# Performance work log

Hardware: AMD Instinct MI355X
Metric: run time of the kernel (lower is better)

Reference implementation:

```python
import jax, jax.numpy as jnp
import numpy as np

# DeformConv hyperparameters (from init_kwargs)
KH, KW = 3, 3
STRIDE, PAD, DIL = 1, 1, 1
GROUPS, DG = 1, 1  # groups=1, deformable_groups=1
B, C, H, W = 4, 64, 128, 128
O = 64
HO = (H + 2 * PAD - (DIL * (KH - 1) + 1)) // STRIDE + 1  # 128
WO = (W + 2 * PAD - (DIL * (KW - 1) + 1)) // STRIDE + 1  # 128


def setup_inputs() -> dict:
    key = jax.random.key(0)
    k1, k2, k3, k4 = jax.random.split(key, 4)
    x = jax.random.normal(k1, (B, C, H, W), dtype=jnp.float32)
    # offset channels: dg * K * 2, ordered (y, x) per kernel tap (DCNv1 CUDA layout)
    offset = jax.random.normal(k2, (B, 2 * DG * KH * KW, HO, WO), dtype=jnp.float32)
    fan_in = C * KH * KW
    weight = jax.random.normal(k3, (O, C // GROUPS, KH, KW), dtype=jnp.float32) / np.sqrt(fan_in)
    bias = jax.random.normal(k4, (O,), dtype=jnp.float32) * 0.01
    return {"x": x, "offset": offset, "weight": weight, "bias": bias}


def _deform_sample(x, offset):
    """Bilinear-sample x at deformed kernel tap locations.
    Returns [B, C, K, HO, WO] where K = KH*KW."""
    K = KH * KW
    Cg = C // DG
    # offset -> [B, DG, K, 2, HO, WO]; channel layout: dg*2*K, pairs (y, x)
    off = offset.reshape(B, DG, K, 2, HO, WO)
    off_y, off_x = off[:, :, :, 0], off[:, :, :, 1]  # [B, DG, K, HO, WO]

    ki = (jnp.arange(K) // KW).astype(jnp.float32)  # kernel row
    kj = (jnp.arange(K) % KW).astype(jnp.float32)   # kernel col
    base_h = (jnp.arange(HO) * STRIDE - PAD).astype(jnp.float32)
    base_w = (jnp.arange(WO) * STRIDE - PAD).astype(jnp.float32)

    # sampling positions [B, DG, K, HO, WO]
    py = off_y + (ki * DIL)[None, None, :, None, None] + base_h[None, None, None, :, None]
    px = off_x + (kj * DIL)[None, None, :, None, None] + base_w[None, None, None, None, :]

    y0f = jnp.floor(py)
    x0f = jnp.floor(px)
    ly = py - y0f
    lx = px - x0f
    hy = 1.0 - ly
    hx = 1.0 - lx
    y0 = y0f.astype(jnp.int32)
    x0 = x0f.astype(jnp.int32)
    y1 = y0 + 1
    x1 = x0 + 1

    flat = x.reshape(B, DG, Cg, H * W)

    def gather(yi, xi, wgt):
        valid = (yi >= 0) & (yi < H) & (xi >= 0) & (xi < W)
        idx = jnp.clip(yi, 0, H - 1) * W + jnp.clip(xi, 0, W - 1)
        idx = idx.reshape(B, DG, 1, K * HO * WO)
        v = jnp.take_along_axis(flat, idx, axis=-1).reshape(B, DG, Cg, K, HO, WO)
        return v * (wgt * valid.astype(wgt.dtype))[:, :, None]

    val = (gather(y0, x0, hy * hx) + gather(y0, x1, hy * lx)
           + gather(y1, x0, ly * hx) + gather(y1, x1, ly * lx))
    return val.reshape(B, C, K, HO, WO)


def reference(x, offset, weight, bias):
    sampled = _deform_sample(x, offset)              # [B, C, K, HO, WO]
    w = weight.reshape(O, C, KH * KW)                # groups = 1
    out = jnp.einsum('bckhw,ock->bohw', sampled, w)  # im2col + GEMM
    return out + bias[None, :, None, None]
```

## Files before the change

kernel.cpp:

```cpp
#include <hip/hip_runtime.h>
#include <hip/hip_fp16.h>


#define B_  4
#define C_  64
#define H_  128
#define W_  128
#define O_  64
#define HO_ 128
#define WO_ 128
#define NCHUNK 8
#define NGW 12
#define KSTEPS 3
#define NT_ 32
#define NTASK (9 * NT_)
#define SG  10
#define SBUF (SG * NT_ * 8)

typedef _Float16 half8 __attribute__((ext_vector_type(8)));
typedef __attribute__((ext_vector_type(4))) float f32x4;

union H8 { float4 v; __half2 h2[4]; half8 v8; };

__global__ __launch_bounds__(256)
void prep(const float* __restrict__ x, const float* __restrict__ w,
          __half* __restrict__ xt, __half* __restrict__ wt) {
    const int tid = threadIdx.x;
    if (blockIdx.x < 2048) {
        int t = blockIdx.x * 256 + tid;
        int xc = t & 127;
        int y  = (t >> 7) & 127;
        int ch = (t >> 14) & 7;
        int b  = t >> 17;
        const float* xp = x + (((size_t)(b * C_ + ch * 8) * H_) + y) * W_ + xc;
        union { __half h[8]; float4 v; } pk;
#pragma unroll
        for (int e = 0; e < 8; ++e) pk.h[e] = __float2half_rn(xp[e * H_ * W_]);
        *(float4*)(xt + (size_t)t * 8) = pk.v;
    } else {
        int t = (blockIdx.x - 2048) * 256 + tid;
        if (t >= NCHUNK * NGW * O_) return;
        int o  = t & 63;
        int g  = (t >> 6) % NGW;
        int ch = (t >> 6) / NGW;
        union { __half h[8]; float4 v; } pk;
#pragma unroll
        for (int e = 0; e < 8; ++e)
            pk.h[e] = (g < 9) ? __float2half_rn(w[(o * C_ + ch * 8 + e) * 9 + g])
                              : __half(0.0f);
        *(float4*)(wt + (size_t)t * 8) = pk.v;
    }
}

__global__ __launch_bounds__(256, 4)
void dcn_mfma(const __half* __restrict__ xt, const float* __restrict__ off,
              const __half* __restrict__ wt, const float* __restrict__ bias,
              float* __restrict__ out) {
    __shared__ __align__(16) _Float16 sS[2 * SBUF];

    const int tid = threadIdx.x;
    const int bid = blockIdx.x;
    const int w4  = bid & 3;
    const int ho  = (bid >> 2) & (HO_ - 1);
    const int b   = bid >> 9;
    const int woB = w4 * NT_;

    int a0_[2], a1_[2];
    __half2 ua2_[2], ub2_[2], va2_[2], vb2_[2];
#pragma unroll
    for (int r = 0; r < 2; ++r) {
        int task = tid + r * 256;
        int tk = (task < NTASK) ? task : 0;
        int k  = tk >> 5;
        int wo = (tk & (NT_ - 1)) + woB;
        int ki = k / 3, kj = k - 3 * ki;
        float oy = off[(((b * 18) + 2 * k    ) * HO_ + ho) * WO_ + wo];
        float ox = off[(((b * 18) + 2 * k + 1) * HO_ + ho) * WO_ + wo];
        float py = (float)(ho - 1 + ki) + oy;
        float px = (float)(wo - 1 + kj) + ox;
        float y0f = floorf(py), x0f = floorf(px);
        int   y0 = (int)y0f,   x0 = (int)x0f;
        float ly = py - y0f,   lx = px - x0f;
        float hy = 1.f - ly,   hx = 1.f - lx;
        int y1 = y0 + 1, x1 = x0 + 1;
        float vy0 = (y0 >= 0 && y0 < H_) ? 1.f : 0.f;
        float vy1 = (y1 >= 0 && y1 < H_) ? 1.f : 0.f;
        float vx0 = (x0 >= 0 && x0 < W_) ? 1.f : 0.f;
        float vx1 = (x1 >= 0 && x1 < W_) ? 1.f : 0.f;
        int cy0 = min(max(y0, 0), H_ - 1), cy1 = min(max(y1, 0), H_ - 1);
        int cx0 = min(max(x0, 0), W_ - 1), cx1 = min(max(x1, 0), W_ - 1);
        int ax  = min(max(x0, 0), W_ - 2);
        float w00 = hy * hx * vy0 * vx0;
        float w01 = hy * lx * vy0 * vx1;
        float w10 = ly * hx * vy1 * vx0;
        float w11 = ly * lx * vy1 * vx1;
        float s0 = (cx0 != ax) ? 1.f : 0.f;
        float s1 = (cx1 != ax) ? 1.f : 0.f;
        a0_[r] = cy0 * W_ + ax;
        a1_[r] = cy1 * W_ + ax;
        ua2_[r] = __float2half2_rn(w00 * (1.f - s0) + w01 * (1.f - s1));
        ub2_[r] = __float2half2_rn(w00 * s0 + w01 * s1);
        va2_[r] = __float2half2_rn(w10 * (1.f - s0) + w11 * (1.f - s1));
        vb2_[r] = __float2half2_rn(w10 * s0 + w11 * s1);
    }

    if (tid < 128) {
        ((unsigned int*)&sS[9 * NT_ * 8])[tid]        = 0u;
        ((unsigned int*)&sS[SBUF + 9 * NT_ * 8])[tid] = 0u;
    }

    H8 q00, q01, q10, q11;
    H8 p00, p01, p10, p11;

    auto issue = [&](int ch) {
        const float4* xc = (const float4*)(xt + ((size_t)(b * NCHUNK + ch)) * (H_ * W_ * 8));
        q00.v = xc[a0_[0]];      q01.v = xc[a0_[0] + 1];
        q10.v = xc[a1_[0]];      q11.v = xc[a1_[0] + 1];
        if (tid < 32) {
            p00.v = xc[a0_[1]];  p01.v = xc[a0_[1] + 1];
            p10.v = xc[a1_[1]];  p11.v = xc[a1_[1] + 1];
        }
    };

    auto blend = [&](int bufi) {
        _Float16* buf = sS + bufi * SBUF;
        {
            int k = tid >> 5, wo = tid & (NT_ - 1);
            H8 s;
#pragma unroll
            for (int j = 0; j < 4; ++j) {
                __half2 t0 = __hmul2(ua2_[0], q00.h2[j]);
                t0 = __hfma2(ub2_[0], q01.h2[j], t0);
                t0 = __hfma2(va2_[0], q10.h2[j], t0);
                t0 = __hfma2(vb2_[0], q11.h2[j], t0);
                s.h2[j] = t0;
            }
            *(half8*)&buf[(k * NT_ + wo) * 8] = s.v8;
        }
        if (tid < 32) {
            int task = tid + 256;
            int k = task >> 5, wo = task & (NT_ - 1);
            H8 s;
#pragma unroll
            for (int j = 0; j < 4; ++j) {
                __half2 t0 = __hmul2(ua2_[1], p00.h2[j]);
                t0 = __hfma2(ub2_[1], p01.h2[j], t0);
                t0 = __hfma2(va2_[1], p10.h2[j], t0);
                t0 = __hfma2(vb2_[1], p11.h2[j], t0);
                s.h2[j] = t0;
            }
            *(half8*)&buf[(k * NT_ + wo) * 8] = s.v8;
        }
    };

    const int lane = tid & 63;
    const int wv   = tid >> 6;
    const int ow   = wv & 1;
    const int nw   = wv >> 1;
    const int quad = lane >> 4;
    const int l15  = lane & 15;

    f32x4 acc[2];
    acc[0] = (f32x4){0.f, 0.f, 0.f, 0.f};
    acc[1] = (f32x4){0.f, 0.f, 0.f, 0.f};

    issue(0);

    for (int ch = 0; ch < NCHUNK; ++ch) {
        blend(ch & 1);
        __syncthreads();
        if (ch + 1 < NCHUNK) issue(ch + 1);

        const __half*   wc  = wt + (size_t)(ch * NGW) * O_ * 8;
        const _Float16* buf = sS + (ch & 1) * SBUF;
#pragma unroll
        for (int ks = 0; ks < KSTEPS; ++ks) {
            int g  = ks * 4 + quad;
            int gb = (g < 9) ? g : 9;
            half8 bfr = *(const half8*)&buf[(gb * NT_ + nw * 16 + l15) * 8];
#pragma unroll
            for (int ot = 0; ot < 2; ++ot) {
                half8 afr = *(const half8*)(wc + (size_t)(g * O_ + ow * 32 + ot * 16 + l15) * 8);
                acc[ot] = __builtin_amdgcn_mfma_f32_16x16x32_f16(afr, bfr, acc[ot], 0, 0, 0);
            }
        }
    }

#pragma unroll
    for (int ot = 0; ot < 2; ++ot) {
        int wo = woB + nw * 16 + l15;
#pragma unroll
        for (int rg = 0; rg < 4; ++rg) {
            int o = ow * 32 + ot * 16 + quad * 4 + rg;
            out[(((size_t)(b * O_ + o)) * HO_ + ho) * WO_ + wo] = acc[ot][rg] + bias[o];
        }
    }
}

extern "C" void kernel_launch(void* const* d_in, const int* in_sizes, int n_in,
                              void* d_out, int out_size, void* d_ws, size_t ws_size,
                              hipStream_t stream) {
    const float* x    = (const float*)d_in[0];
    const float* off  = (const float*)d_in[1];
    const float* w    = (const float*)d_in[2];
    const float* bias = (const float*)d_in[3];
    float* out = (float*)d_out;

    __half* wt = (__half*)d_ws;
    __half* xt = (__half*)((char*)d_ws + 262144);

    hipLaunchKernelGGL(prep, dim3(2048 + 24), dim3(256), 0, stream, x, w, xt, wt);
    hipLaunchKernelGGL(dcn_mfma, dim3(B_ * HO_ * (WO_ / NT_)), dim3(256), 0, stream,
                       xt, off, wt, bias, out);
}
```

Before: 107.2 us.

## Stage input tile in LDS for bilinear gathers and software-pipeline MFMA

Each block now cooperatively loads a 16x48 pixel tile of the fp16 channel-packed input into shared memory with coalesced loads. The bilinear corner gathers read from that tile, falling back to global memory only when a sample lands outside it. The main loop is restructured so each chunk's sampling overlaps with the MFMA work of the previous chunk. This trades scattered global gathers for more LDS traffic, an extra barrier per chunk, added shared memory (lower occupancy risk) and divergent fallback paths.

After: 101.1 us. -5.7%, faster.

```diff
diff --git a/kernel.cpp b/kernel.cpp
--- a/kernel.cpp
+++ b/kernel.cpp
@@ -16,6 +16,9 @@
 #define NTASK (9 * NT_)
 #define SG  10
 #define SBUF (SG * NT_ * 8)
+#define TR  16
+#define TC  48
+#define TSLOTS (TR * TC)
 
 typedef _Float16 half8 __attribute__((ext_vector_type(8)));
 typedef __attribute__((ext_vector_type(4))) float f32x4;
@@ -57,6 +60,7 @@
               const __half* __restrict__ wt, const float* __restrict__ bias,
               float* __restrict__ out) {
     __shared__ __align__(16) _Float16 sS[2 * SBUF];
+    __shared__ __align__(16) _Float16 sT[TSLOTS * 8];
 
     const int tid = threadIdx.x;
     const int bid = blockIdx.x;
@@ -64,8 +68,10 @@
     const int ho  = (bid >> 2) & (HO_ - 1);
     const int b   = bid >> 9;
     const int woB = w4 * NT_;
-
-    int a0_[2], a1_[2];
+    const int yb  = ho - 7;
+    const int xb  = woB - 8;
+
+    int ty0_[2], ty1_[2], tx_[2], fb_[2];
     __half2 ua2_[2], ub2_[2], va2_[2], vb2_[2];
 #pragma unroll
     for (int r = 0; r < 2; ++r) {
@@ -96,60 +102,74 @@
         float w11 = ly * lx * vy1 * vx1;
         float s0 = (cx0 != ax) ? 1.f : 0.f;
         float s1 = (cx1 != ax) ? 1.f : 0.f;
-        a0_[r] = cy0 * W_ + ax;
-        a1_[r] = cy1 * W_ + ax;
+        ty0_[r] = cy0 - yb;
+        ty1_[r] = cy1 - yb;
+        tx_[r]  = ax - xb;
+        fb_[r]  = ((unsigned)ty0_[r] > (unsigned)(TR - 1)) |
+                  ((unsigned)ty1_[r] > (unsigned)(TR - 1)) |
+                  ((unsigned)tx_[r]  > (unsigned)(TC - 2));
         ua2_[r] = __float2half2_rn(w00 * (1.f - s0) + w01 * (1.f - s1));
         ub2_[r] = __float2half2_rn(w00 * s0 + w01 * s1);
         va2_[r] = __float2half2_rn(w10 * (1.f - s0) + w11 * (1.f - s1));
         vb2_[r] = __float2half2_rn(w10 * s0 + w11 * s1);
     }
 
+    int gofs[3];
+#pragma unroll
+    for (int j = 0; j < 3; ++j) {
+        int s  = tid + j * 256;
+        int rr = s / TC, cc = s - rr * TC;
+        int yc = min(max(yb + rr, 0), H_ - 1);
+        int xc = min(max(xb + cc, 0), W_ - 1);
+        gofs[j] = yc * W_ + xc;
+    }
+
     if (tid < 128) {
         ((unsigned int*)&sS[9 * NT_ * 8])[tid]        = 0u;
         ((unsigned int*)&sS[SBUF + 9 * NT_ * 8])[tid] = 0u;
     }
 
-    H8 q00, q01, q10, q11;
-    H8 p00, p01, p10, p11;
-
+    float4 pf0, pf1, pf2;
     auto issue = [&](int ch) {
         const float4* xc = (const float4*)(xt + ((size_t)(b * NCHUNK + ch)) * (H_ * W_ * 8));
-        q00.v = xc[a0_[0]];      q01.v = xc[a0_[0] + 1];
-        q10.v = xc[a1_[0]];      q11.v = xc[a1_[0] + 1];
-        if (tid < 32) {
-            p00.v = xc[a0_[1]];  p01.v = xc[a0_[1] + 1];
-            p10.v = xc[a1_[1]];  p11.v = xc[a1_[1] + 1];
-        }
+        pf0 = xc[gofs[0]];
+        pf1 = xc[gofs[1]];
+        pf2 = xc[gofs[2]];
     };
 
-    auto blend = [&](int bufi) {
-        _Float16* buf = sS + bufi * SBUF;
-        {
-            int k = tid >> 5, wo = tid & (NT_ - 1);
-            H8 s;
-#pragma unroll
-            for (int j = 0; j < 4; ++j) {
-                __half2 t0 = __hmul2(ua2_[0], q00.h2[j]);
-                t0 = __hfma2(ub2_[0], q01.h2[j], t0);
-                t0 = __hfma2(va2_[0], q10.h2[j], t0);
-                t0 = __hfma2(vb2_[0], q11.h2[j], t0);
-                s.h2[j] = t0;
+    auto sample = [&](int ch) {
+        _Float16* buf = sS + (ch & 1) * SBUF;
+        const float4* xcg = (const float4*)(xt + ((size_t)(b * NCHUNK + ch)) * (H_ * W_ * 8));
+        const float4* tl  = (const float4*)sT;
+#pragma unroll
+        for (int r = 0; r < 2; ++r) {
+            int task = tid + r * 256;
+            if (task < NTASK) {
+                int k  = task >> 5;
+                int wo = task & (NT_ - 1);
+                H8 q00, q01, q10, q11;
+                if (!fb_[r]) {
+                    int a0 = ty0_[r] * TC + tx_[r];
+                    int a1 = ty1_[r] * TC + tx_[r];
+                    q00.v = tl[a0];  q01.v = tl[a0 + 1];
+                    q10.v = tl[a1];  q11.v = tl[a1 + 1];
+                } else {
+                    int a0 = (ty0_[r] + yb) * W_ + (tx_[r] + xb);
+                    int a1 = (ty1_[r] + yb) * W_ + (tx_[r] + xb);
+                    q00.v = xcg[a0]; q01.v = xcg[a0 + 1];
+                    q10.v = xcg[a1]; q11.v = xcg[a1 + 1];
+                }
+                H8 s;
+#pragma unroll
+                for (int j = 0; j < 4; ++j) {
+                    __half2 t0 = __hmul2(ua2_[r], q00.h2[j]);
+                    t0 = __hfma2(ub2_[r], q01.h2[j], t0);
+                    t0 = __hfma2(va2_[r], q10.h2[j], t0);
+                    t0 = __hfma2(vb2_[r], q11.h2[j], t0);
+                    s.h2[j] = t0;
+                }
+                *(half8*)&buf[(k * NT_ + wo) * 8] = s.v8;
             }
-            *(half8*)&buf[(k * NT_ + wo) * 8] = s.v8;
-        }
-        if (tid < 32) {
-            int task = tid + 256;
-            int k = task >> 5, wo = task & (NT_ - 1);
-            H8 s;
-#pragma unroll
-            for (int j = 0; j < 4; ++j) {
-                __half2 t0 = __hmul2(ua2_[1], p00.h2[j]);
-                t0 = __hfma2(ub2_[1], p01.h2[j], t0);
-                t0 = __hfma2(va2_[1], p10.h2[j], t0);
-                t0 = __hfma2(vb2_[1], p11.h2[j], t0);
-                s.h2[j] = t0;
-            }
-            *(half8*)&buf[(k * NT_ + wo) * 8] = s.v8;
         }
     };
 
@@ -164,13 +184,7 @@
     acc[0] = (f32x4){0.f, 0.f, 0.f, 0.f};
     acc[1] = (f32x4){0.f, 0.f, 0.f, 0.f};
 
-    issue(0);
-
-    for (int ch = 0; ch < NCHUNK; ++ch) {
-        blend(ch & 1);
-        __syncthreads();
-        if (ch + 1 < NCHUNK) issue(ch + 1);
-
+    auto mfma_chunk = [&](int ch) {
         const __half*   wc  = wt + (size_t)(ch * NGW) * O_ * 8;
         const _Float16* buf = sS + (ch & 1) * SBUF;
 #pragma unroll
@@ -184,7 +198,21 @@
                 acc[ot] = __builtin_amdgcn_mfma_f32_16x16x32_f16(afr, bfr, acc[ot], 0, 0, 0);
             }
         }
-    }
+    };
+
+    issue(0);
+    for (int ch = 0; ch < NCHUNK; ++ch) {
+        float4* tw = (float4*)sT;
+        tw[tid]       = pf0;
+        tw[tid + 256] = pf1;
+        tw[tid + 512] = pf2;
+        __syncthreads();
+        if (ch + 1 < NCHUNK) issue(ch + 1);
+        sample(ch);
+        if (ch > 0) mfma_chunk(ch - 1);
+        __syncthreads();
+    }
+    mfma_chunk(NCHUNK - 1);
 
 #pragma unroll
     for (int ot = 0; ot < 2; ++ot) {
```

## Stage input tile in LDS and blend bilinear samples directly into MFMA fragments

Applied to the files above, without the earlier changes.

Each block now cooperatively loads a 16x48 halo tile of the fp16 input into shared memory for every channel chunk. Bilinear gathers read from that tile, and fall back to global memory when the deformed sample lands outside it. Each lane blends its own B-fragment in registers instead of writing blended samples to shared memory, and the block shrinks to 128 threads with each wave covering all 64 outputs. The aim is to cut scattered global gathers, but it adds a second barrier per chunk and moves the tile load out of a double buffer. Divergent fallback loads are frequent, since random offsets often leave the 16-row window.

Measured after the change: 151.9 us. +41.7%, slower.

```diff
diff --git a/kernel.cpp b/kernel.cpp
--- a/kernel.cpp
+++ b/kernel.cpp
@@ -9,18 +9,19 @@
 #define O_  64
 #define HO_ 128
 #define WO_ 128
+#define HW_ (H_ * W_)
 #define NCHUNK 8
 #define NGW 12
 #define KSTEPS 3
 #define NT_ 32
-#define NTASK (9 * NT_)
-#define SG  10
-#define SBUF (SG * NT_ * 8)
+#define TR  16
+#define TC  48
+#define TSLOTS (TR * TC)
 
 typedef _Float16 half8 __attribute__((ext_vector_type(8)));
 typedef __attribute__((ext_vector_type(4))) float f32x4;
 
-union H8 { float4 v; __half2 h2[4]; half8 v8; };
+union H8 { float4 v; __half2 h2[4]; half8 v8; __half h[8]; };
 
 __global__ __launch_bounds__(256)
 void prep(const float* __restrict__ x, const float* __restrict__ w,
@@ -35,7 +36,7 @@
         const float* xp = x + (((size_t)(b * C_ + ch * 8) * H_) + y) * W_ + xc;
         union { __half h[8]; float4 v; } pk;
 #pragma unroll
-        for (int e = 0; e < 8; ++e) pk.h[e] = __float2half_rn(xp[e * H_ * W_]);
+        for (int e = 0; e < 8; ++e) pk.h[e] = __float2half_rn(xp[e * HW_]);
         *(float4*)(xt + (size_t)t * 8) = pk.v;
     } else {
         int t = (blockIdx.x - 2048) * 256 + tid;
@@ -52,11 +53,11 @@
     }
 }
 
-__global__ __launch_bounds__(256, 4)
+__global__ __launch_bounds__(128, 4)
 void dcn_mfma(const __half* __restrict__ xt, const float* __restrict__ off,
               const __half* __restrict__ wt, const float* __restrict__ bias,
               float* __restrict__ out) {
-    __shared__ __align__(16) _Float16 sS[2 * SBUF];
+    __shared__ __align__(16) _Float16 sT[TSLOTS * 8];
 
     const int tid = threadIdx.x;
     const int bid = blockIdx.x;
@@ -64,20 +65,27 @@
     const int ho  = (bid >> 2) & (HO_ - 1);
     const int b   = bid >> 9;
     const int woB = w4 * NT_;
-
-    int a0_[2], a1_[2];
-    __half2 ua2_[2], ub2_[2], va2_[2], vb2_[2];
-#pragma unroll
-    for (int r = 0; r < 2; ++r) {
-        int task = tid + r * 256;
-        int tk = (task < NTASK) ? task : 0;
-        int k  = tk >> 5;
-        int wo = (tk & (NT_ - 1)) + woB;
+    const int yorg = ho - 7;
+    const int xorg = woB - 8;
+
+    const int lane = tid & 63;
+    const int nw   = tid >> 6;
+    const int quad = lane >> 4;
+    const int l15  = lane & 15;
+    const int wo_l = woB + nw * 16 + l15;
+
+    int a0_[3], a1_[3], fb_[3];
+    __half2 ua2_[3], ub2_[3], va2_[3], vb2_[3];
+#pragma unroll
+    for (int j = 0; j < 3; ++j) {
+        int g = j * 4 + quad;
+        int valid = (g < 9);
+        int k  = valid ? g : 0;
         int ki = k / 3, kj = k - 3 * ki;
-        float oy = off[(((b * 18) + 2 * k    ) * HO_ + ho) * WO_ + wo];
-        float ox = off[(((b * 18) + 2 * k + 1) * HO_ + ho) * WO_ + wo];
+        float oy = off[(((b * 18) + 2 * k    ) * HO_ + ho) * WO_ + wo_l];
+        float ox = off[(((b * 18) + 2 * k + 1) * HO_ + ho) * WO_ + wo_l];
         float py = (float)(ho - 1 + ki) + oy;
-        float px = (float)(wo - 1 + kj) + ox;
+        float px = (float)(wo_l - 1 + kj) + ox;
         float y0f = floorf(py), x0f = floorf(px);
         int   y0 = (int)y0f,   x0 = (int)x0f;
         float ly = py - y0f,   lx = px - x0f;
@@ -90,109 +98,99 @@
         int cy0 = min(max(y0, 0), H_ - 1), cy1 = min(max(y1, 0), H_ - 1);
         int cx0 = min(max(x0, 0), W_ - 1), cx1 = min(max(x1, 0), W_ - 1);
         int ax  = min(max(x0, 0), W_ - 2);
-        float w00 = hy * hx * vy0 * vx0;
-        float w01 = hy * lx * vy0 * vx1;
-        float w10 = ly * hx * vy1 * vx0;
-        float w11 = ly * lx * vy1 * vx1;
+        float en  = valid ? 1.f : 0.f;
+        float w00 = hy * hx * vy0 * vx0 * en;
+        float w01 = hy * lx * vy0 * vx1 * en;
+        float w10 = ly * hx * vy1 * vx0 * en;
+        float w11 = ly * lx * vy1 * vx1 * en;
         float s0 = (cx0 != ax) ? 1.f : 0.f;
         float s1 = (cx1 != ax) ? 1.f : 0.f;
-        a0_[r] = cy0 * W_ + ax;
-        a1_[r] = cy1 * W_ + ax;
-        ua2_[r] = __float2half2_rn(w00 * (1.f - s0) + w01 * (1.f - s1));
-        ub2_[r] = __float2half2_rn(w00 * s0 + w01 * s1);
-        va2_[r] = __float2half2_rn(w10 * (1.f - s0) + w11 * (1.f - s1));
-        vb2_[r] = __float2half2_rn(w10 * s0 + w11 * s1);
-    }
-
-    if (tid < 128) {
-        ((unsigned int*)&sS[9 * NT_ * 8])[tid]        = 0u;
-        ((unsigned int*)&sS[SBUF + 9 * NT_ * 8])[tid] = 0u;
-    }
-
-    H8 q00, q01, q10, q11;
-    H8 p00, p01, p10, p11;
-
+        int ty0 = cy0 - yorg, ty1 = cy1 - yorg, tx = ax - xorg;
+        int fb = ((unsigned)ty0 > (unsigned)(TR - 1)) |
+                 ((unsigned)ty1 > (unsigned)(TR - 1)) |
+                 ((unsigned)tx  > (unsigned)(TC - 2));
+        fb_[j] = valid ? fb : 0;
+        a0_[j] = fb ? (cy0 * W_ + ax) : (ty0 * TC + tx);
+        a1_[j] = fb ? (cy1 * W_ + ax) : (ty1 * TC + tx);
+        ua2_[j] = __float2half2_rn(w00 * (1.f - s0) + w01 * (1.f - s1));
+        ub2_[j] = __float2half2_rn(w00 * s0 + w01 * s1);
+        va2_[j] = __float2half2_rn(w10 * (1.f - s0) + w11 * (1.f - s1));
+        vb2_[j] = __float2half2_rn(w10 * s0 + w11 * s1);
+    }
+
+    int gofs[6];
+#pragma unroll
+    for (int j = 0; j < 6; ++j) {
+        int s  = tid + j * 128;
+        int rr = s / TC, cc = s - rr * TC;
+        int yc = min(max(yorg + rr, 0), H_ - 1);
+        int xc = min(max(xorg + cc, 0), W_ - 1);
+        gofs[j] = yc * W_ + xc;
+    }
+
+    float4 pf[6];
     auto issue = [&](int ch) {
-        const float4* xc = (const float4*)(xt + ((size_t)(b * NCHUNK + ch)) * (H_ * W_ * 8));
-        q00.v = xc[a0_[0]];      q01.v = xc[a0_[0] + 1];
-        q10.v = xc[a1_[0]];      q11.v = xc[a1_[0] + 1];
-        if (tid < 32) {
-            p00.v = xc[a0_[1]];  p01.v = xc[a0_[1] + 1];
-            p10.v = xc[a1_[1]];  p11.v = xc[a1_[1] + 1];
-        }
+        const float4* xc = (const float4*)(xt + ((size_t)(b * NCHUNK + ch)) * (HW_ * 8));
+#pragma unroll
+        for (int j = 0; j < 6; ++j) pf[j] = xc[gofs[j]];
     };
 
-    auto blend = [&](int bufi) {
-        _Float16* buf = sS + bufi * SBUF;
-        {
-            int k = tid >> 5, wo = tid & (NT_ - 1);
-            H8 s;
-#pragma unroll
-            for (int j = 0; j < 4; ++j) {
-                __half2 t0 = __hmul2(ua2_[0], q00.h2[j]);
-                t0 = __hfma2(ub2_[0], q01.h2[j], t0);
-                t0 = __hfma2(va2_[0], q10.h2[j], t0);
-                t0 = __hfma2(vb2_[0], q11.h2[j], t0);
-                s.h2[j] = t0;
-            }
-            *(half8*)&buf[(k * NT_ + wo) * 8] = s.v8;
-        }
-        if (tid < 32) {
-            int task = tid + 256;
-            int k = task >> 5, wo = task & (NT_ - 1);
-            H8 s;
-#pragma unroll
-            for (int j = 0; j < 4; ++j) {
-                __half2 t0 = __hmul2(ua2_[1], p00.h2[j]);
-                t0 = __hfma2(ub2_[1], p01.h2[j], t0);
-                t0 = __hfma2(va2_[1], p10.h2[j], t0);
-                t0 = __hfma2(vb2_[1], p11.h2[j], t0);
-                s.h2[j] = t0;
-            }
-            *(half8*)&buf[(k * NT_ + wo) * 8] = s.v8;
-        }
-    };
-
-    const int lane = tid & 63;
-    const int wv   = tid >> 6;
-    const int ow   = wv & 1;
-    const int nw   = wv >> 1;
-    const int quad = lane >> 4;
-    const int l15  = lane & 15;
-
-    f32x4 acc[2];
-    acc[0] = (f32x4){0.f, 0.f, 0.f, 0.f};
-    acc[1] = (f32x4){0.f, 0.f, 0.f, 0.f};
+    f32x4 acc[4];
+#pragma unroll
+    for (int ot = 0; ot < 4; ++ot) acc[ot] = (f32x4){0.f, 0.f, 0.f, 0.f};
 
     issue(0);
-
     for (int ch = 0; ch < NCHUNK; ++ch) {
-        blend(ch & 1);
+        float4* tw = (float4*)sT;
+#pragma unroll
+        for (int j = 0; j < 6; ++j) tw[tid + j * 128] = pf[j];
         __syncthreads();
         if (ch + 1 < NCHUNK) issue(ch + 1);
 
-        const __half*   wc  = wt + (size_t)(ch * NGW) * O_ * 8;
-        const _Float16* buf = sS + (ch & 1) * SBUF;
+        half8 bf[3];
+        const float4* tl = (const float4*)sT;
+        const float4* xcg = (const float4*)(xt + ((size_t)(b * NCHUNK + ch)) * (HW_ * 8));
+#pragma unroll
+        for (int j = 0; j < 3; ++j) {
+            H8 q00, q01, q10, q11;
+            if (!fb_[j]) {
+                q00.v = tl[a0_[j]];  q01.v = tl[a0_[j] + 1];
+                q10.v = tl[a1_[j]];  q11.v = tl[a1_[j] + 1];
+            } else {
+                q00.v = xcg[a0_[j]]; q01.v = xcg[a0_[j] + 1];
+                q10.v = xcg[a1_[j]]; q11.v = xcg[a1_[j] + 1];
+            }
+            H8 s;
+#pragma unroll
+            for (int p = 0; p < 4; ++p) {
+                __half2 t0 = __hmul2(ua2_[j], q00.h2[p]);
+                t0 = __hfma2(ub2_[j], q01.h2[p], t0);
+                t0 = __hfma2(va2_[j], q10.h2[p], t0);
+                t0 = __hfma2(vb2_[j], q11.h2[p], t0);
+                s.h2[p] = t0;
+            }
+            bf[j] = s.v8;
+        }
+        __syncthreads();
+
+        const __half* wc = wt + (size_t)(ch * NGW) * O_ * 8;
 #pragma unroll
         for (int ks = 0; ks < KSTEPS; ++ks) {
-            int g  = ks * 4 + quad;
-            int gb = (g < 9) ? g : 9;
-            half8 bfr = *(const half8*)&buf[(gb * NT_ + nw * 16 + l15) * 8];
-#pragma unroll
-            for (int ot = 0; ot < 2; ++ot) {
-                half8 afr = *(const half8*)(wc + (size_t)(g * O_ + ow * 32 + ot * 16 + l15) * 8);
-                acc[ot] = __builtin_amdgcn_mfma_f32_16x16x32_f16(afr, bfr, acc[ot], 0, 0, 0);
+            int g = ks * 4 + quad;
+#pragma unroll
+            for (int ot = 0; ot < 4; ++ot) {
+                half8 afr = *(const half8*)(wc + (size_t)(g * O_ + ot * 16 + l15) * 8);
+                acc[ot] = __builtin_amdgcn_mfma_f32_16x16x32_f16(afr, bf[ks], acc[ot], 0, 0, 0);
             }
         }
     }
 
 #pragma unroll
-    for (int ot = 0; ot < 2; ++ot) {
-        int wo = woB + nw * 16 + l15;
+    for (int ot = 0; ot < 4; ++ot) {
 #pragma unroll
         for (int rg = 0; rg < 4; ++rg) {
-            int o = ow * 32 + ot * 16 + quad * 4 + rg;
-            out[(((size_t)(b * O_ + o)) * HO_ + ho) * WO_ + wo] = acc[ot][rg] + bias[o];
+            int o = ot * 16 + quad * 4 + rg;
+            out[(((size_t)(b * O_ + o)) * HO_ + ho) * WO_ + wo_l] = acc[ot][rg] + bias[o];
         }
     }
 }
@@ -210,6 +208,6 @@
     __half* xt = (__half*)((char*)d_ws + 262144);
 
     hipLaunchKernelGGL(prep, dim3(2048 + 24), dim3(256), 0, stream, x, w, xt, wt);
-    hipLaunchKernelGGL(dcn_mfma, dim3(B_ * HO_ * (WO_ / NT_)), dim3(256), 0, stream,
+    hipLaunchKernelGGL(dcn_mfma, dim3(B_ * HO_ * (WO_ / NT_)), dim3(128), 0, stream,
                        xt, off, wt, bias, out);
 }
```
